# Kernel tuning notes

Hardware: AMD Instinct MI355X
Metric: run time of the kernel (lower is better)

Reference implementation:

```python
import jax, jax.numpy as jnp
import numpy as np

N_NODES = 100000
N_EDGES = 1250000
IN_DIM = 6
HID = 64


def gcn_conv(x, W, b, src, dst, deg_inv_sqrt):
    # x: [N, F_in] -> [N, F_out]; symmetric-normalized aggregation with self-loops
    h = x @ W  # [N, F_out]
    norm = deg_inv_sqrt[src] * deg_inv_sqrt[dst]  # [E]
    msg = h[src] * norm[:, None]                  # gather + scale, [E, F_out]
    agg = jax.ops.segment_sum(msg, dst, num_segments=x.shape[0])
    # self-loop contribution: norm = deg_inv_sqrt[i]^2 = 1/deg[i]
    out = agg + h * (deg_inv_sqrt ** 2)[:, None] + b
    return out


def setup_inputs() -> dict:
    key = jax.random.key(0)
    ks = jax.random.split(key, 8)
    x = jax.random.normal(ks[0], (N_NODES, IN_DIM), dtype=jnp.float32)
    edge_index = jax.random.randint(ks[1], (2, N_EDGES), 0, N_NODES, dtype=jnp.int64)
    s1 = 1.0 / np.sqrt(IN_DIM)
    s2 = 1.0 / np.sqrt(HID)
    W1 = jax.random.uniform(ks[2], (IN_DIM, HID), jnp.float32, -s1, s1)
    b1 = jnp.zeros((HID,), jnp.float32)
    W2 = jax.random.uniform(ks[3], (HID, HID), jnp.float32, -s2, s2)
    b2 = jnp.zeros((HID,), jnp.float32)
    Wfc = jax.random.uniform(ks[4], (HID, 1), jnp.float32, -s2, s2)
    bfc = jnp.zeros((1,), jnp.float32)
    return {"x": x, "edge_index": edge_index, "W1": W1, "b1": b1,
            "W2": W2, "b2": b2, "Wfc": Wfc, "bfc": bfc}


def reference(x, edge_index, W1, b1, W2, b2, Wfc, bfc):
    src, dst = edge_index[0], edge_index[1]
    n = x.shape[0]
    # degree with self-loops (GCN default): in-degree at destination + 1
    deg = jax.ops.segment_sum(jnp.ones((src.shape[0],), x.dtype), dst, num_segments=n) + 1.0
    deg_inv_sqrt = jax.lax.rsqrt(deg)
    h = gcn_conv(x, W1, b1, src, dst, deg_inv_sqrt)
    h = jax.nn.relu(h)
    h = gcn_conv(h, W2, b2, src, dst, deg_inv_sqrt)
    g = h.mean(axis=0)              # [HID] graph readout
    out = jax.nn.sigmoid(g @ Wfc + bfc)  # [1]
    return out
```

## Files before the change

### kernel.cpp

```cpp
#include <hip/hip_runtime.h>
#include <math.h>

#define N_NODES 100000
#define N_EDGES 1250000
#define IN_DIM 6
#define HID 64

#define BIN_SHIFT 8
#define BIN_NODES 256
#define NBIN 391
#define A_BLOCKS 250
#define EPB (N_EDGES / A_BLOCKS)
#define CAP 4096
#define SOFF (NBIN * CAP)

__device__ inline float lo16(unsigned u) { return __uint_as_float(u << 16); }
__device__ inline float hi16(unsigned u) { return __uint_as_float(u & 0xffff0000u); }
__device__ inline unsigned short f2bf(float f) {
    unsigned u = __float_as_uint(f);
    u += 0x7FFFu + ((u >> 16) & 1u);
    return (unsigned short)(u >> 16);
}
__device__ inline unsigned pack2(float a, float b) {
    return (unsigned)f2bf(a) | ((unsigned)f2bf(b) << 16);
}

__global__ __launch_bounds__(1024) void binFill(const int* __restrict__ src,
                                                const int* __restrict__ dst,
                                                int* __restrict__ cnt,
                                                unsigned* __restrict__ rec) {
    __shared__ int lc[2 * NBIN];
    __shared__ int lb[2 * NBIN];
    int t = threadIdx.x;
    for (int i = t; i < 2 * NBIN; i += 1024) lc[i] = 0;
    __syncthreads();
    int base = blockIdx.x * EPB;
    for (int i0 = t * 4; i0 < EPB; i0 += 4096) {
        int4 d4 = *(const int4*)&dst[base + i0];
        int4 s4 = *(const int4*)&src[base + i0];
        atomicAdd(&lc[d4.x >> BIN_SHIFT], 1);
        atomicAdd(&lc[d4.y >> BIN_SHIFT], 1);
        atomicAdd(&lc[d4.z >> BIN_SHIFT], 1);
        atomicAdd(&lc[d4.w >> BIN_SHIFT], 1);
        atomicAdd(&lc[NBIN + (s4.x >> BIN_SHIFT)], 1);
        atomicAdd(&lc[NBIN + (s4.y >> BIN_SHIFT)], 1);
        atomicAdd(&lc[NBIN + (s4.z >> BIN_SHIFT)], 1);
        atomicAdd(&lc[NBIN + (s4.w >> BIN_SHIFT)], 1);
    }
    __syncthreads();
    for (int i = t; i < 2 * NBIN; i += 1024) {
        int c = lc[i];
        int off = (c > 0) ? atomicAdd(&cnt[i], c) : 0;
        int bin = (i < NBIN) ? i : (i - NBIN);
        lb[i] = ((i < NBIN) ? bin * CAP : SOFF + bin * CAP) + off;
        lc[i] = 0;
    }
    __syncthreads();
    for (int i0 = t * 4; i0 < EPB; i0 += 4096) {
        int4 d4 = *(const int4*)&dst[base + i0];
        int4 s4 = *(const int4*)&src[base + i0];
        int bD0 = d4.x >> BIN_SHIFT, bD1 = d4.y >> BIN_SHIFT;
        int bD2 = d4.z >> BIN_SHIFT, bD3 = d4.w >> BIN_SHIFT;
        int p0 = lb[bD0] + atomicAdd(&lc[bD0], 1);
        int p1 = lb[bD1] + atomicAdd(&lc[bD1], 1);
        int p2 = lb[bD2] + atomicAdd(&lc[bD2], 1);
        int p3 = lb[bD3] + atomicAdd(&lc[bD3], 1);
        rec[p0] = ((unsigned)(d4.x & (BIN_NODES - 1)) << 17) | (unsigned)s4.x;
        rec[p1] = ((unsigned)(d4.y & (BIN_NODES - 1)) << 17) | (unsigned)s4.y;
        rec[p2] = ((unsigned)(d4.z & (BIN_NODES - 1)) << 17) | (unsigned)s4.z;
        rec[p3] = ((unsigned)(d4.w & (BIN_NODES - 1)) << 17) | (unsigned)s4.w;
        int bS0 = NBIN + (s4.x >> BIN_SHIFT), bS1 = NBIN + (s4.y >> BIN_SHIFT);
        int bS2 = NBIN + (s4.z >> BIN_SHIFT), bS3 = NBIN + (s4.w >> BIN_SHIFT);
        int q0 = lb[bS0] + atomicAdd(&lc[bS0], 1);
        int q1 = lb[bS1] + atomicAdd(&lc[bS1], 1);
        int q2 = lb[bS2] + atomicAdd(&lc[bS2], 1);
        int q3 = lb[bS3] + atomicAdd(&lc[bS3], 1);
        rec[q0] = ((unsigned)(s4.x & (BIN_NODES - 1)) << 17) | (unsigned)d4.x;
        rec[q1] = ((unsigned)(s4.y & (BIN_NODES - 1)) << 17) | (unsigned)d4.y;
        rec[q2] = ((unsigned)(s4.z & (BIN_NODES - 1)) << 17) | (unsigned)d4.z;
        rec[q3] = ((unsigned)(s4.w & (BIN_NODES - 1)) << 17) | (unsigned)d4.w;
    }
}

__global__ __launch_bounds__(1024) void disXH(const unsigned* __restrict__ rec,
                                              const int* __restrict__ cnt,
                                              const float* __restrict__ x,
                                              int* __restrict__ deg,
                                              float* __restrict__ dis,
                                              uint4* __restrict__ xpad) {
    __shared__ int histS[4][BIN_NODES];
    int t = threadIdx.x, g = t >> 8;
    if (t < 4 * BIN_NODES) ((int*)histS)[t] = 0;
    __syncthreads();
    int bin = blockIdx.x;
    int beg = bin * CAP, c = cnt[bin];
    int nv = c & ~3;
    for (int j = t * 4; j < nv; j += 4096) {
        uint4 r4 = *(const uint4*)&rec[beg + j];
        atomicAdd(&histS[g][r4.x >> 17], 1);
        atomicAdd(&histS[g][r4.y >> 17], 1);
        atomicAdd(&histS[g][r4.z >> 17], 1);
        atomicAdd(&histS[g][r4.w >> 17], 1);
    }
    for (int j = nv + t; j < c; j += 1024) atomicAdd(&histS[g][rec[beg + j] >> 17], 1);
    __syncthreads();
    if (t < BIN_NODES) {
        int n = (bin << BIN_SHIFT) + t;
        if (n < N_NODES) {
            int h = histS[0][t] + histS[1][t] + histS[2][t] + histS[3][t];
            deg[n] = h;
            float d = rsqrtf((float)h + 1.0f);
            dis[n] = d;
            float2 xa = *(const float2*)&x[n * IN_DIM + 0];
            float2 xb = *(const float2*)&x[n * IN_DIM + 2];
            float2 xc = *(const float2*)&x[n * IN_DIM + 4];
            uint4 u;
            u.x = pack2(xa.x * d, xa.y * d);
            u.y = pack2(xb.x * d, xb.y * d);
            u.z = pack2(xc.x * d, xc.y * d);
            u.w = 0;
            xpad[n] = u;
        }
    }
}

__global__ __launch_bounds__(1024) void aggW(const unsigned* __restrict__ rec,
                                             const int* __restrict__ cnt,
                                             const int* __restrict__ deg,
                                             const float* __restrict__ dis,
                                             const uint4* __restrict__ xpad,
                                             const float* __restrict__ W1,
                                             const float* __restrict__ b1,
                                             const float* __restrict__ W2,
                                             const float* __restrict__ b2,
                                             const float* __restrict__ Wfc,
                                             const float* __restrict__ bfc,
                                             float* __restrict__ vsum,
                                             int* __restrict__ done,
                                             float* __restrict__ out) {
    __shared__ unsigned srcL[CAP];
    __shared__ float wlS[4][BIN_NODES];
    __shared__ int degL[BIN_NODES];
    __shared__ int startS[BIN_NODES];
    __shared__ int cur[BIN_NODES];
    __shared__ int sc[BIN_NODES];
    __shared__ float sAll[BIN_NODES][8];
    __shared__ float w1s[IN_DIM * HID];
    __shared__ float b1s[HID];
    __shared__ float vpart[HID];
    __shared__ int isLast;
    int t = threadIdx.x, g = t >> 8;
    int bin = blockIdx.x;

    if (t < 4 * BIN_NODES) ((float*)wlS)[t] = 0.f;
    if (t < IN_DIM * HID) w1s[t] = W1[t];
    if (t >= 1024 - HID) { int c = t - (1024 - HID); b1s[c] = b1[c]; vpart[c] = 0.f; }
    __syncthreads();

    {
        int beg = SOFF + bin * CAP, c = cnt[NBIN + bin];
        int nv = c & ~3;
        for (int j = t * 4; j < nv; j += 4096) {
            uint4 r4 = *(const uint4*)&rec[beg + j];
            atomicAdd(&wlS[g][r4.x >> 17], dis[r4.x & 131071u]);
            atomicAdd(&wlS[g][r4.y >> 17], dis[r4.y & 131071u]);
            atomicAdd(&wlS[g][r4.z >> 17], dis[r4.z & 131071u]);
            atomicAdd(&wlS[g][r4.w >> 17], dis[r4.w & 131071u]);
        }
        for (int j = nv + t; j < c; j += 1024) {
            unsigned r = rec[beg + j];
            atomicAdd(&wlS[g][r >> 17], dis[r & 131071u]);
        }
    }
    __syncthreads();

    if (t < BIN_NODES) {
        int n = (bin << BIN_SHIFT) + t;
        int h = (n < N_NODES) ? deg[n] : 0;
        degL[t] = h;
        sc[t] = h;
        float d = (n < N_NODES) ? rsqrtf((float)h + 1.0f) : 0.f;
        float wloc = wlS[0][t] + wlS[1][t] + wlS[2][t] + wlS[3][t];
        sAll[t][6] = d;
        sAll[t][7] = (n < N_NODES) ? d * (wloc + d) : 0.f;
    }
    __syncthreads();
    for (int off = 1; off < BIN_NODES; off <<= 1) {
        int add = 0;
        if (t < BIN_NODES && t >= off) add = sc[t - off];
        __syncthreads();
        if (t < BIN_NODES) sc[t] += add;
        __syncthreads();
    }
    if (t < BIN_NODES) {
        int st = sc[t] - degL[t];
        startS[t] = st;
        cur[t] = st;
    }
    __syncthreads();

    {
        int beg = bin * CAP, c = cnt[bin];
        int nv = c & ~3;
        for (int j = t * 4; j < nv; j += 4096) {
            uint4 r4 = *(const uint4*)&rec[beg + j];
            int p0 = atomicAdd(&cur[r4.x >> 17], 1);
            int p1 = atomicAdd(&cur[r4.y >> 17], 1);
            int p2 = atomicAdd(&cur[r4.z >> 17], 1);
            int p3 = atomicAdd(&cur[r4.w >> 17], 1);
            if (p0 < CAP) srcL[p0] = r4.x & 131071u;
            if (p1 < CAP) srcL[p1] = r4.y & 131071u;
            if (p2 < CAP) srcL[p2] = r4.z & 131071u;
            if (p3 < CAP) srcL[p3] = r4.w & 131071u;
        }
        for (int j = nv + t; j < c; j += 1024) {
            unsigned r = rec[beg + j];
            int pos = atomicAdd(&cur[r >> 17], 1);
            if (pos < CAP) srcL[pos] = r & 131071u;
        }
    }
    __syncthreads();

    {
        int node = t >> 2, sub = t & 3;
        int st = startS[node], cn = degL[node];
        int lim = min(st + cn, CAP);
        float s0 = 0.f, s1 = 0.f, s2 = 0.f, s3 = 0.f, s4 = 0.f, s5 = 0.f;
        for (int k = st + sub; k < lim; k += 4) {
            uint4 px = xpad[srcL[k]];
            s0 += lo16(px.x); s1 += hi16(px.x);
            s2 += lo16(px.y); s3 += hi16(px.y);
            s4 += lo16(px.z); s5 += hi16(px.z);
        }
        s0 += __shfl_xor(s0, 1, 64); s0 += __shfl_xor(s0, 2, 64);
        s1 += __shfl_xor(s1, 1, 64); s1 += __shfl_xor(s1, 2, 64);
        s2 += __shfl_xor(s2, 1, 64); s2 += __shfl_xor(s2, 2, 64);
        s3 += __shfl_xor(s3, 1, 64); s3 += __shfl_xor(s3, 2, 64);
        s4 += __shfl_xor(s4, 1, 64); s4 += __shfl_xor(s4, 2, 64);
        s5 += __shfl_xor(s5, 1, 64); s5 += __shfl_xor(s5, 2, 64);
        if (sub == 0) {
            int n = (bin << BIN_SHIFT) + node;
            if (n < N_NODES) {
                uint4 px = xpad[n];
                s0 += lo16(px.x); s1 += hi16(px.x);
                s2 += lo16(px.y); s3 += hi16(px.y);
                s4 += lo16(px.z); s5 += hi16(px.z);
            }
            sAll[node][0] = s0; sAll[node][1] = s1; sAll[node][2] = s2;
            sAll[node][3] = s3; sAll[node][4] = s4; sAll[node][5] = s5;
        }
    }
    __syncthreads();

    {
        int c = t & 63, grp = t >> 6;
        float v = 0.f;
#pragma unroll
        for (int i = 0; i < 16; ++i) {
            int node = grp * 16 + i;
            float d = sAll[node][6], cw = sAll[node][7];
            float a = sAll[node][0] * w1s[0 * HID + c]
                    + sAll[node][1] * w1s[1 * HID + c]
                    + sAll[node][2] * w1s[2 * HID + c]
                    + sAll[node][3] * w1s[3 * HID + c]
                    + sAll[node][4] * w1s[4 * HID + c]
                    + sAll[node][5] * w1s[5 * HID + c];
            v += cw * fmaxf(d * a + b1s[c], 0.f);
        }
        atomicAdd(&vpart[c], v);
    }
    __syncthreads();
    if (t < HID) atomicAdd(&vsum[t], vpart[t]);

    if (t == 0) {
        __threadfence();
        int ticket = atomicAdd(done, 1);
        isLast = (ticket == NBIN - 1);
    }
    __syncthreads();
    if (isLast) {
        if (t < HID) vpart[t] = atomicAdd(&vsum[t], 0.f) * (1.0f / N_NODES);
        __syncthreads();
        if (t < HID) {
            float gg = b2[t];
            for (int k = 0; k < HID; ++k) gg += vpart[k] * W2[k * HID + t];
            float z = gg * Wfc[t];
            for (int off = 32; off > 0; off >>= 1) z += __shfl_down(z, off, 64);
            if (t == 0) out[0] = 1.0f / (1.0f + expf(-(z + bfc[0])));
        }
    }
}

extern "C" void kernel_launch(void* const* d_in, const int* in_sizes, int n_in,
                              void* d_out, int out_size, void* d_ws, size_t ws_size,
                              hipStream_t stream) {
    const float* x   = (const float*)d_in[0];
    const int*   ei  = (const int*)d_in[1];
    const float* W1  = (const float*)d_in[2];
    const float* b1  = (const float*)d_in[3];
    const float* W2  = (const float*)d_in[4];
    const float* b2  = (const float*)d_in[5];
    const float* Wfc = (const float*)d_in[6];
    const float* bfc = (const float*)d_in[7];
    const int* src = ei;
    const int* dst = ei + N_EDGES;

    char* ws = (char*)d_ws;
    size_t off = 0;
    auto alloc = (+[](char* base, size_t* o, size_t bytes) {
        char* p = base + *o;
        *o += (bytes + 255) & ~(size_t)255;
        return p;
    });
    int*      cnt  = (int*)     alloc(ws, &off, (size_t)2 * NBIN * 4);
    float*    vsum = (float*)   alloc(ws, &off, 64 * 4);
    int*      done = (int*)     alloc(ws, &off, 256);
    uint4*    xpad = (uint4*)   alloc(ws, &off, (size_t)N_NODES * 16);
    float*    dis  = (float*)   alloc(ws, &off, (size_t)N_NODES * 4);
    int*      deg  = (int*)     alloc(ws, &off, (size_t)N_NODES * 4);
    unsigned* rec  = (unsigned*)alloc(ws, &off, (size_t)2 * SOFF * 4);

    hipMemsetAsync(cnt, 0, 3840, stream);

    binFill<<<A_BLOCKS, 1024, 0, stream>>>(src, dst, cnt, rec);
    disXH<<<NBIN, 1024, 0, stream>>>(rec, cnt, x, deg, dis, xpad);
    aggW<<<NBIN, 1024, 0, stream>>>(rec, cnt, deg, dis, xpad, W1, b1, W2, b2,
                                    Wfc, bfc, vsum, done, (float*)d_out);
}
```

Before: 126.7 us.

## Rebin nodes into 512 bins with per-slot sub-buckets to spread global atomics

```diff
diff --git a/kernel.cpp b/kernel.cpp
--- a/kernel.cpp
+++ b/kernel.cpp
@@ -6,12 +6,14 @@
 #define IN_DIM 6
 #define HID 64
 
-#define BIN_SHIFT 8
-#define BIN_NODES 256
-#define NBIN 391
+#define BIN_N 196
+#define NBIN 512
+#define BPAD 256
 #define A_BLOCKS 250
 #define EPB (N_EDGES / A_BLOCKS)
-#define CAP 4096
+#define NSLOT 4
+#define SLOTCAP 1024
+#define CAP (NSLOT * SLOTCAP)
 #define SOFF (NBIN * CAP)
 
 __device__ inline float lo16(unsigned u) { return __uint_as_float(u << 16); }
@@ -32,53 +34,53 @@
     __shared__ int lc[2 * NBIN];
     __shared__ int lb[2 * NBIN];
     int t = threadIdx.x;
+    int slot = blockIdx.x & (NSLOT - 1);
     for (int i = t; i < 2 * NBIN; i += 1024) lc[i] = 0;
     __syncthreads();
     int base = blockIdx.x * EPB;
     for (int i0 = t * 4; i0 < EPB; i0 += 4096) {
         int4 d4 = *(const int4*)&dst[base + i0];
         int4 s4 = *(const int4*)&src[base + i0];
-        atomicAdd(&lc[d4.x >> BIN_SHIFT], 1);
-        atomicAdd(&lc[d4.y >> BIN_SHIFT], 1);
-        atomicAdd(&lc[d4.z >> BIN_SHIFT], 1);
-        atomicAdd(&lc[d4.w >> BIN_SHIFT], 1);
-        atomicAdd(&lc[NBIN + (s4.x >> BIN_SHIFT)], 1);
-        atomicAdd(&lc[NBIN + (s4.y >> BIN_SHIFT)], 1);
-        atomicAdd(&lc[NBIN + (s4.z >> BIN_SHIFT)], 1);
-        atomicAdd(&lc[NBIN + (s4.w >> BIN_SHIFT)], 1);
+        atomicAdd(&lc[d4.x / BIN_N], 1);
+        atomicAdd(&lc[d4.y / BIN_N], 1);
+        atomicAdd(&lc[d4.z / BIN_N], 1);
+        atomicAdd(&lc[d4.w / BIN_N], 1);
+        atomicAdd(&lc[NBIN + s4.x / BIN_N], 1);
+        atomicAdd(&lc[NBIN + s4.y / BIN_N], 1);
+        atomicAdd(&lc[NBIN + s4.z / BIN_N], 1);
+        atomicAdd(&lc[NBIN + s4.w / BIN_N], 1);
     }
     __syncthreads();
     for (int i = t; i < 2 * NBIN; i += 1024) {
         int c = lc[i];
-        int off = (c > 0) ? atomicAdd(&cnt[i], c) : 0;
+        int chain = (i < NBIN) ? 0 : 1;
         int bin = (i < NBIN) ? i : (i - NBIN);
-        lb[i] = ((i < NBIN) ? bin * CAP : SOFF + bin * CAP) + off;
+        int off = (c > 0) ? atomicAdd(&cnt[(slot * 2 + chain) * NBIN + bin], c) : 0;
+        lb[i] = ((chain == 0) ? 0 : SOFF) + bin * CAP + slot * SLOTCAP + off;
         lc[i] = 0;
     }
     __syncthreads();
     for (int i0 = t * 4; i0 < EPB; i0 += 4096) {
         int4 d4 = *(const int4*)&dst[base + i0];
         int4 s4 = *(const int4*)&src[base + i0];
-        int bD0 = d4.x >> BIN_SHIFT, bD1 = d4.y >> BIN_SHIFT;
-        int bD2 = d4.z >> BIN_SHIFT, bD3 = d4.w >> BIN_SHIFT;
+        int bD0 = d4.x / BIN_N, bD1 = d4.y / BIN_N, bD2 = d4.z / BIN_N, bD3 = d4.w / BIN_N;
         int p0 = lb[bD0] + atomicAdd(&lc[bD0], 1);
         int p1 = lb[bD1] + atomicAdd(&lc[bD1], 1);
         int p2 = lb[bD2] + atomicAdd(&lc[bD2], 1);
         int p3 = lb[bD3] + atomicAdd(&lc[bD3], 1);
-        rec[p0] = ((unsigned)(d4.x & (BIN_NODES - 1)) << 17) | (unsigned)s4.x;
-        rec[p1] = ((unsigned)(d4.y & (BIN_NODES - 1)) << 17) | (unsigned)s4.y;
-        rec[p2] = ((unsigned)(d4.z & (BIN_NODES - 1)) << 17) | (unsigned)s4.z;
-        rec[p3] = ((unsigned)(d4.w & (BIN_NODES - 1)) << 17) | (unsigned)s4.w;
-        int bS0 = NBIN + (s4.x >> BIN_SHIFT), bS1 = NBIN + (s4.y >> BIN_SHIFT);
-        int bS2 = NBIN + (s4.z >> BIN_SHIFT), bS3 = NBIN + (s4.w >> BIN_SHIFT);
-        int q0 = lb[bS0] + atomicAdd(&lc[bS0], 1);
-        int q1 = lb[bS1] + atomicAdd(&lc[bS1], 1);
-        int q2 = lb[bS2] + atomicAdd(&lc[bS2], 1);
-        int q3 = lb[bS3] + atomicAdd(&lc[bS3], 1);
-        rec[q0] = ((unsigned)(s4.x & (BIN_NODES - 1)) << 17) | (unsigned)d4.x;
-        rec[q1] = ((unsigned)(s4.y & (BIN_NODES - 1)) << 17) | (unsigned)d4.y;
-        rec[q2] = ((unsigned)(s4.z & (BIN_NODES - 1)) << 17) | (unsigned)d4.z;
-        rec[q3] = ((unsigned)(s4.w & (BIN_NODES - 1)) << 17) | (unsigned)d4.w;
+        rec[p0] = ((unsigned)(d4.x - bD0 * BIN_N) << 17) | (unsigned)s4.x;
+        rec[p1] = ((unsigned)(d4.y - bD1 * BIN_N) << 17) | (unsigned)s4.y;
+        rec[p2] = ((unsigned)(d4.z - bD2 * BIN_N) << 17) | (unsigned)s4.z;
+        rec[p3] = ((unsigned)(d4.w - bD3 * BIN_N) << 17) | (unsigned)s4.w;
+        int bS0 = s4.x / BIN_N, bS1 = s4.y / BIN_N, bS2 = s4.z / BIN_N, bS3 = s4.w / BIN_N;
+        int q0 = lb[NBIN + bS0] + atomicAdd(&lc[NBIN + bS0], 1);
+        int q1 = lb[NBIN + bS1] + atomicAdd(&lc[NBIN + bS1], 1);
+        int q2 = lb[NBIN + bS2] + atomicAdd(&lc[NBIN + bS2], 1);
+        int q3 = lb[NBIN + bS3] + atomicAdd(&lc[NBIN + bS3], 1);
+        rec[q0] = ((unsigned)(s4.x - bS0 * BIN_N) << 17) | (unsigned)d4.x;
+        rec[q1] = ((unsigned)(s4.y - bS1 * BIN_N) << 17) | (unsigned)d4.y;
+        rec[q2] = ((unsigned)(s4.z - bS2 * BIN_N) << 17) | (unsigned)d4.z;
+        rec[q3] = ((unsigned)(s4.w - bS3 * BIN_N) << 17) | (unsigned)d4.w;
     }
 }
 
@@ -88,24 +90,20 @@
                                               int* __restrict__ deg,
                                               float* __restrict__ dis,
                                               uint4* __restrict__ xpad) {
-    __shared__ int histS[4][BIN_NODES];
-    int t = threadIdx.x, g = t >> 8;
-    if (t < 4 * BIN_NODES) ((int*)histS)[t] = 0;
-    __syncthreads();
+    __shared__ int histS[NSLOT][BPAD];
+    int t = threadIdx.x, g = t >> 8, lt = t & 255;
     int bin = blockIdx.x;
-    int beg = bin * CAP, c = cnt[bin];
-    int nv = c & ~3;
-    for (int j = t * 4; j < nv; j += 4096) {
-        uint4 r4 = *(const uint4*)&rec[beg + j];
-        atomicAdd(&histS[g][r4.x >> 17], 1);
-        atomicAdd(&histS[g][r4.y >> 17], 1);
-        atomicAdd(&histS[g][r4.z >> 17], 1);
-        atomicAdd(&histS[g][r4.w >> 17], 1);
-    }
-    for (int j = nv + t; j < c; j += 1024) atomicAdd(&histS[g][rec[beg + j] >> 17], 1);
-    __syncthreads();
-    if (t < BIN_NODES) {
-        int n = (bin << BIN_SHIFT) + t;
+    for (int i = lt; i < BPAD; i += 256) histS[g][i] = 0;
+    __syncthreads();
+    {
+        int c = cnt[(g * 2 + 0) * NBIN + bin];
+        int beg = bin * CAP + g * SLOTCAP;
+        for (int j = beg + lt; j < beg + c; j += 256)
+            atomicAdd(&histS[g][rec[j] >> 17], 1);
+    }
+    __syncthreads();
+    if (t < BIN_N) {
+        int n = bin * BIN_N + t;
         if (n < N_NODES) {
             int h = histS[0][t] + histS[1][t] + histS[2][t] + histS[3][t];
             deg[n] = h;
@@ -139,60 +137,54 @@
                                              int* __restrict__ done,
                                              float* __restrict__ out) {
     __shared__ unsigned srcL[CAP];
-    __shared__ float wlS[4][BIN_NODES];
-    __shared__ int degL[BIN_NODES];
-    __shared__ int startS[BIN_NODES];
-    __shared__ int cur[BIN_NODES];
-    __shared__ int sc[BIN_NODES];
-    __shared__ float sAll[BIN_NODES][8];
+    __shared__ float wlS[NSLOT][BPAD];
+    __shared__ int degL[BPAD];
+    __shared__ int startS[BPAD];
+    __shared__ int cur[BPAD];
+    __shared__ int sc[BPAD];
+    __shared__ float sAll[BPAD][8];
     __shared__ float w1s[IN_DIM * HID];
     __shared__ float b1s[HID];
     __shared__ float vpart[HID];
     __shared__ int isLast;
-    int t = threadIdx.x, g = t >> 8;
+    int t = threadIdx.x, g = t >> 8, lt = t & 255;
     int bin = blockIdx.x;
 
-    if (t < 4 * BIN_NODES) ((float*)wlS)[t] = 0.f;
+    for (int i = lt; i < BPAD; i += 256) wlS[g][i] = 0.f;
     if (t < IN_DIM * HID) w1s[t] = W1[t];
     if (t >= 1024 - HID) { int c = t - (1024 - HID); b1s[c] = b1[c]; vpart[c] = 0.f; }
     __syncthreads();
 
     {
-        int beg = SOFF + bin * CAP, c = cnt[NBIN + bin];
-        int nv = c & ~3;
-        for (int j = t * 4; j < nv; j += 4096) {
-            uint4 r4 = *(const uint4*)&rec[beg + j];
-            atomicAdd(&wlS[g][r4.x >> 17], dis[r4.x & 131071u]);
-            atomicAdd(&wlS[g][r4.y >> 17], dis[r4.y & 131071u]);
-            atomicAdd(&wlS[g][r4.z >> 17], dis[r4.z & 131071u]);
-            atomicAdd(&wlS[g][r4.w >> 17], dis[r4.w & 131071u]);
-        }
-        for (int j = nv + t; j < c; j += 1024) {
-            unsigned r = rec[beg + j];
+        int c = cnt[(g * 2 + 1) * NBIN + bin];
+        int beg = SOFF + bin * CAP + g * SLOTCAP;
+        for (int j = beg + lt; j < beg + c; j += 256) {
+            unsigned r = rec[j];
             atomicAdd(&wlS[g][r >> 17], dis[r & 131071u]);
         }
     }
     __syncthreads();
 
-    if (t < BIN_NODES) {
-        int n = (bin << BIN_SHIFT) + t;
-        int h = (n < N_NODES) ? deg[n] : 0;
+    if (t < BPAD) {
+        int n = bin * BIN_N + t;
+        bool valid = (t < BIN_N) && (n < N_NODES);
+        int h = valid ? deg[n] : 0;
         degL[t] = h;
         sc[t] = h;
-        float d = (n < N_NODES) ? rsqrtf((float)h + 1.0f) : 0.f;
+        float d = valid ? rsqrtf((float)h + 1.0f) : 0.f;
         float wloc = wlS[0][t] + wlS[1][t] + wlS[2][t] + wlS[3][t];
         sAll[t][6] = d;
-        sAll[t][7] = (n < N_NODES) ? d * (wloc + d) : 0.f;
-    }
-    __syncthreads();
-    for (int off = 1; off < BIN_NODES; off <<= 1) {
+        sAll[t][7] = valid ? d * (wloc + d) : 0.f;
+    }
+    __syncthreads();
+    for (int off = 1; off < BPAD; off <<= 1) {
         int add = 0;
-        if (t < BIN_NODES && t >= off) add = sc[t - off];
+        if (t < BPAD && t >= off) add = sc[t - off];
         __syncthreads();
-        if (t < BIN_NODES) sc[t] += add;
+        if (t < BPAD) sc[t] += add;
         __syncthreads();
     }
-    if (t < BIN_NODES) {
+    if (t < BPAD) {
         int st = sc[t] - degL[t];
         startS[t] = st;
         cur[t] = st;
@@ -200,21 +192,10 @@
     __syncthreads();
 
     {
-        int beg = bin * CAP, c = cnt[bin];
-        int nv = c & ~3;
-        for (int j = t * 4; j < nv; j += 4096) {
-            uint4 r4 = *(const uint4*)&rec[beg + j];
-            int p0 = atomicAdd(&cur[r4.x >> 17], 1);
-            int p1 = atomicAdd(&cur[r4.y >> 17], 1);
-            int p2 = atomicAdd(&cur[r4.z >> 17], 1);
-            int p3 = atomicAdd(&cur[r4.w >> 17], 1);
-            if (p0 < CAP) srcL[p0] = r4.x & 131071u;
-            if (p1 < CAP) srcL[p1] = r4.y & 131071u;
-            if (p2 < CAP) srcL[p2] = r4.z & 131071u;
-            if (p3 < CAP) srcL[p3] = r4.w & 131071u;
-        }
-        for (int j = nv + t; j < c; j += 1024) {
-            unsigned r = rec[beg + j];
+        int c = cnt[(g * 2 + 0) * NBIN + bin];
+        int beg = bin * CAP + g * SLOTCAP;
+        for (int j = beg + lt; j < beg + c; j += 256) {
+            unsigned r = rec[j];
             int pos = atomicAdd(&cur[r >> 17], 1);
             if (pos < CAP) srcL[pos] = r & 131071u;
         }
@@ -239,8 +220,8 @@
         s4 += __shfl_xor(s4, 1, 64); s4 += __shfl_xor(s4, 2, 64);
         s5 += __shfl_xor(s5, 1, 64); s5 += __shfl_xor(s5, 2, 64);
         if (sub == 0) {
-            int n = (bin << BIN_SHIFT) + node;
-            if (n < N_NODES) {
+            int n = bin * BIN_N + node;
+            if (node < BIN_N && n < N_NODES) {
                 uint4 px = xpad[n];
                 s0 += lo16(px.x); s1 += hi16(px.x);
                 s2 += lo16(px.y); s3 += hi16(px.y);
@@ -312,7 +293,7 @@
         *o += (bytes + 255) & ~(size_t)255;
         return p;
     });
-    int*      cnt  = (int*)     alloc(ws, &off, (size_t)2 * NBIN * 4);
+    int*      cnt  = (int*)     alloc(ws, &off, (size_t)NSLOT * 2 * NBIN * 4);
     float*    vsum = (float*)   alloc(ws, &off, 64 * 4);
     int*      done = (int*)     alloc(ws, &off, 256);
     uint4*    xpad = (uint4*)   alloc(ws, &off, (size_t)N_NODES * 16);
@@ -320,7 +301,7 @@
     int*      deg  = (int*)     alloc(ws, &off, (size_t)N_NODES * 4);
     unsigned* rec  = (unsigned*)alloc(ws, &off, (size_t)2 * SOFF * 4);
 
-    hipMemsetAsync(cnt, 0, 3840, stream);
+    hipMemsetAsync(cnt, 0, NSLOT * 2 * NBIN * 4 + 512, stream);
 
     binFill<<<A_BLOCKS, 1024, 0, stream>>>(src, dst, cnt, rec);
     disXH<<<NBIN, 1024, 0, stream>>>(rec, cnt, x, deg, dis, xpad);
```

New measurement: 132.4 us. 1.05x slower.
